# Optimization experiments

Hardware: AMD Instinct MI355X
Metric: run time of the kernel (lower is better)

The kernel has to match this reference:

```python
import jax, jax.numpy as jnp
import numpy as np

WINDOW_SIZES = (4, 16, 64)
MEMORY_DIM = 256


def setup_inputs() -> dict:
    key = jax.random.key(0)
    ks = jax.random.split(key, 9)
    d_model, mem = 256, MEMORY_DIM
    s_in = 1.0 / np.sqrt(d_model)
    s_mem = 1.0 / np.sqrt(mem)
    return {
        "hidden_states": jax.random.normal(ks[0], (2, 4096, d_model), dtype=jnp.float32),
        # weights stored as (in, out) so projection is x @ W + b
        "Wq": jax.random.normal(ks[1], (d_model, mem), dtype=jnp.float32) * s_in,
        "bq": jax.random.normal(ks[2], (mem,), dtype=jnp.float32) * 0.02,
        "Wk": jax.random.normal(ks[3], (d_model, mem), dtype=jnp.float32) * s_in,
        "bk": jax.random.normal(ks[4], (mem,), dtype=jnp.float32) * 0.02,
        "Wv": jax.random.normal(ks[5], (d_model, mem), dtype=jnp.float32) * s_in,
        "bv": jax.random.normal(ks[6], (mem,), dtype=jnp.float32) * 0.02,
        "Wo": jax.random.normal(ks[7], (mem, d_model), dtype=jnp.float32) * s_mem,
        "bo": jax.random.normal(ks[8], (d_model,), dtype=jnp.float32) * 0.02,
    }


def _gather_patches(h, window):
    # h: (B, L, D). Causal window of `window` positions ending at each l,
    # zero-padded on the left (matches F.pad + unfold in the torch module).
    B, L, D = h.shape
    w = min(window, L)
    padded = jnp.pad(h, ((0, 0), (w - 1, 0), (0, 0)))  # (B, L+w-1, D)
    idx = jnp.arange(L)[:, None] + jnp.arange(w)[None, :]  # (L, w)
    return padded[:, idx]  # (B, L, w, D)


def reference(hidden_states, Wq, bq, Wk, bk, Wv, bv, Wo, bo):
    scale = 1.0 / np.sqrt(MEMORY_DIM)
    q = hidden_states @ Wq + bq  # (B, L, M)
    contexts = []
    for window in WINDOW_SIZES:
        patches = _gather_patches(hidden_states, window)  # (B, L, w, D)
        keys = patches @ Wk + bk      # (B, L, w, M)
        values = patches @ Wv + bv    # (B, L, w, M)
        scores = jnp.einsum('bld,blwd->blw', q, keys) * scale
        attn = jax.nn.softmax(scores, axis=-1)
        contexts.append(jnp.einsum('blw,blwd->bld', attn, values))
    merged = contexts[0]
    for c in contexts[1:]:
        merged = merged + c
    merged = merged / len(contexts)
    return hidden_states + merged @ Wo + bo
```

## Files before the change

### kernel.cpp

```cpp
#include <hip/hip_runtime.h>
#include <hip/hip_bf16.h>

#define D 256
#define NROWS 8192
#define LXV 4176
#define VPAD 64
#define KXFB 1064960

#define QBLK 16
#define SSTR 84
#define PSTR 104
#define MSTR 264
#define BSTR 264

typedef unsigned int u32;
typedef unsigned short u16;

typedef short bf16x8 __attribute__((ext_vector_type(8)));
typedef float f32x4 __attribute__((ext_vector_type(4)));

__device__ __forceinline__ u16 f2bf(float f) {
    u32 x = __float_as_uint(f);
    x += 0x7fffu + ((x >> 16) & 1u);
    return (u16)(x >> 16);
}
__device__ __forceinline__ u32 pk2(float a, float b) {
    return (u32)f2bf(a) | ((u32)f2bf(b) << 16);
}

__global__ __launch_bounds__(256) void qkv_mfma(
    const float* __restrict__ H,
    const float* __restrict__ Wq, const float* __restrict__ Wk,
    const float* __restrict__ Wv, const float* __restrict__ Wo,
    const float* __restrict__ bq, const float* __restrict__ bkb,
    const float* __restrict__ bvb,
    u16* __restrict__ Qf, u16* __restrict__ Kxf, u16* __restrict__ Vt,
    u16* __restrict__ WoTf)
{
    __shared__ u16 As[64 * 256];
    __shared__ u16 Bs[64 * BSTR];
    __shared__ u16 Eb[64 * 72];

    const int tid = threadIdx.x;
    const int bx = blockIdx.x;
    const int by = blockIdx.y;
    const int mat = bx >> 2;
    const int n0 = (bx & 3) * 64;
    const int row0 = by * 256;
    const int batch = by >> 4;
    const int lrow0 = row0 & 4095;
    const float* __restrict__ W = (mat == 0) ? Wq : (mat == 1) ? Wk : Wv;
    const float* __restrict__ bias = (mat == 0) ? bq : (mat == 1) ? bkb : bvb;

    const int lane = tid & 63, w = tid >> 6;
    const int l15 = lane & 15, lhi = lane >> 4;
    const int rt2 = (w & 1) * 2, ct2 = (w >> 1) * 2;

    {
        const int kp = tid & 31, ng = tid >> 5;
        u32* bd = (u32*)Bs;
        #pragma unroll
        for (int s = 0; s < 4; ++s) {
            const float* wr = W + (size_t)(s * 64 + 2 * kp) * 256 + n0 + ng * 8;
            float4 a0 = *(const float4*)(wr);
            float4 a1 = *(const float4*)(wr + 4);
            float4 b0 = *(const float4*)(wr + 256);
            float4 b1 = *(const float4*)(wr + 260);
            bd[(ng * 8 + 0) * 132 + s * 32 + kp] = pk2(a0.x, b0.x);
            bd[(ng * 8 + 1) * 132 + s * 32 + kp] = pk2(a0.y, b0.y);
            bd[(ng * 8 + 2) * 132 + s * 32 + kp] = pk2(a0.z, b0.z);
            bd[(ng * 8 + 3) * 132 + s * 32 + kp] = pk2(a0.w, b0.w);
            bd[(ng * 8 + 4) * 132 + s * 32 + kp] = pk2(a1.x, b1.x);
            bd[(ng * 8 + 5) * 132 + s * 32 + kp] = pk2(a1.y, b1.y);
            bd[(ng * 8 + 6) * 132 + s * 32 + kp] = pk2(a1.z, b1.z);
            bd[(ng * 8 + 7) * 132 + s * 32 + kp] = pk2(a1.w, b1.w);
        }
    }
    {
        const int r = tid >> 2, cb = (tid & 3) * 64;
        const float* hp = H + (size_t)(row0 + r) * 256 + cb;
        const int swz = (r & 7) << 3;
        #pragma unroll
        for (int i = 0; i < 16; ++i) {
            float4 h4 = *(const float4*)(hp + i * 4);
            uint2 pv; pv.x = pk2(h4.x, h4.y); pv.y = pk2(h4.z, h4.w);
            *(uint2*)(As + ((r * 256 + cb + i * 4) ^ swz)) = pv;
        }
    }
    __syncthreads();

    for (int t = 0; t < 4; ++t) {
        f32x4 acc[2][2];
        #pragma unroll
        for (int rr = 0; rr < 2; ++rr)
            #pragma unroll
            for (int cc = 0; cc < 2; ++cc)
                acc[rr][cc] = (f32x4){0.f, 0.f, 0.f, 0.f};
        #pragma unroll
        for (int rr = 0; rr < 2; ++rr) {
            const int rowa = (rt2 + rr) * 16 + l15;
            const int swa = (rowa & 7) << 3;
            bf16x8 af[8];
            #pragma unroll
            for (int ks = 0; ks < 8; ++ks)
                af[ks] = *(const bf16x8*)(As + ((rowa * 256 + ks * 32 + lhi * 8) ^ swa));
            #pragma unroll
            for (int ks = 0; ks < 8; ++ks)
                #pragma unroll
                for (int cc = 0; cc < 2; ++cc) {
                    bf16x8 bf = *(const bf16x8*)&Bs[((ct2 + cc) * 16 + l15) * BSTR + ks * 32 + lhi * 8];
                    acc[rr][cc] = __builtin_amdgcn_mfma_f32_16x16x32_bf16(af[ks], bf, acc[rr][cc], 0, 0, 0);
                }
        }
        __syncthreads();

        if (mat == 2) {
            #pragma unroll
            for (int cc = 0; cc < 2; ++cc) {
                const int dl = (ct2 + cc) * 16 + l15;
                const float bi = bvb[n0 + dl];
                #pragma unroll
                for (int rr = 0; rr < 2; ++rr)
                    #pragma unroll
                    for (int reg = 0; reg < 4; ++reg)
                        Eb[dl * 72 + (rt2 + rr) * 16 + lhi * 4 + reg] = f2bf(acc[rr][cc][reg] + bi);
            }
        } else {
            #pragma unroll
            for (int cc = 0; cc < 2; ++cc) {
                const int cl = (ct2 + cc) * 16 + l15;
                const float bi = bias[n0 + cl];
                #pragma unroll
                for (int rr = 0; rr < 2; ++rr)
                    #pragma unroll
                    for (int reg = 0; reg < 4; ++reg)
                        Eb[((rt2 + rr) * 16 + lhi * 4 + reg) * 72 + cl] = f2bf(acc[rr][cc][reg] + bi);
            }
        }
        if (t < 3) {
            const int r = tid >> 2, cb = (tid & 3) * 64;
            const float* hp = H + (size_t)(row0 + (t + 1) * 64 + r) * 256 + cb;
            const int swz = (r & 7) << 3;
            #pragma unroll
            for (int i = 0; i < 16; ++i) {
                float4 h4 = *(const float4*)(hp + i * 4);
                uint2 pv; pv.x = pk2(h4.x, h4.y); pv.y = pk2(h4.z, h4.w);
                *(uint2*)(As + ((r * 256 + cb + i * 4) ^ swz)) = pv;
            }
        }
        __syncthreads();

        if (mat == 2) {
            const int d2 = tid >> 2, q = tid & 3;
            uint4 v0 = *(const uint4*)&Eb[d2 * 72 + q * 16];
            uint4 v1 = *(const uint4*)&Eb[d2 * 72 + q * 16 + 8];
            u16* dst = Vt + ((size_t)batch * 256 + n0 + d2) * LXV + VPAD + lrow0 + t * 64 + q * 16;
            *(uint4*)dst = v0;
            *(uint4*)(dst + 8) = v1;
        } else {
            const int r2 = tid >> 2, c16 = (tid & 3) * 16;
            int rtile, rl;
            u16* base;
            if (mat == 0) {
                const int grow = row0 + t * 64 + r2;
                rtile = grow >> 4; rl = grow & 15;
                base = Qf;
            } else {
                const int prow = VPAD + lrow0 + t * 64 + r2;
                rtile = prow >> 4; rl = prow & 15;
                base = Kxf + (size_t)batch * KXFB;
            }
            #pragma unroll
            for (int h = 0; h < 2; ++h) {
                const int gcol = n0 + c16 + h * 8;
                const int ksq = gcol >> 5;
                const int lhq = (gcol >> 3) & 3;
                uint4 v = *(const uint4*)&Eb[r2 * 72 + c16 + h * 8];
                *(uint4*)&base[((size_t)rtile * 8 + ksq) * 512 + (rl * 4 + lhq) * 8] = v;
            }
        }
    }

    if (bx == 0 && by < 16) {
        float* Tf = (float*)As;
        const int tr = by >> 2, tc = by & 3;
        __syncthreads();
        {
            const int r = tid >> 2, c0 = (tid & 3) * 16;
            const float* src = Wo + (size_t)(tr * 64 + r) * 256 + tc * 64 + c0;
            #pragma unroll
            for (int i = 0; i < 4; ++i) {
                float4 v = *(const float4*)(src + i * 4);
                Tf[r * 68 + c0 + i * 4 + 0] = v.x;
                Tf[r * 68 + c0 + i * 4 + 1] = v.y;
                Tf[r * 68 + c0 + i * 4 + 2] = v.z;
                Tf[r * 68 + c0 + i * 4 + 3] = v.w;
            }
        }
        __syncthreads();
        {
            const int n = tid >> 2, k0 = (tid & 3) * 16;
            const int gcol = tc * 64 + n;
            const int colt = gcol >> 4, cl = gcol & 15;
            const int gk = tr * 64 + k0;
            const int ksw = gk >> 5;
            const int lhw = (gk >> 3) & 3;
            u32 pw[8];
            #pragma unroll
            for (int i = 0; i < 8; ++i)
                pw[i] = pk2(Tf[(k0 + 2 * i) * 68 + n], Tf[(k0 + 2 * i + 1) * 68 + n]);
            u16* base = WoTf + ((size_t)colt * 8 + ksw) * 512 + (cl * 4 + lhw) * 8;
            *(uint4*)base = *(uint4*)&pw[0];
            *(uint4*)(base + 8) = *(uint4*)&pw[4];
        }
    }
    if (bx == 4 && (by & 15) == 0) {
        const int batch2 = by >> 4;
        const int ks = tid >> 5, u = tid & 31;
        const u16 val = f2bf(bkb[ks * 32 + u]);
        u16* base = Kxf + (size_t)batch2 * KXFB;
        #pragma unroll
        for (int pt = 0; pt < 4; ++pt)
            #pragma unroll
            for (int rl = 0; rl < 16; ++rl)
                base[((size_t)pt * 8 + ks) * 512 + rl * 32 + u] = val;
    }
    if (bx == 8 && (by & 15) == 0) {
        const int batch2 = by >> 4;
        const u16 val = f2bf(bvb[tid]);
        const u32 vv = (u32)val | ((u32)val << 16);
        uint4 o; o.x = vv; o.y = vv; o.z = vv; o.w = vv;
        u16* dst = Vt + ((size_t)batch2 * 256 + tid) * LXV;
        #pragma unroll
        for (int j = 0; j < 8; ++j) *(uint4*)(dst + j * 8) = o;
    }
}

__global__ __launch_bounds__(256) void attn_out(
    const u16* __restrict__ Qf, const u16* __restrict__ Kxf,
    const u16* __restrict__ Vt, const u16* __restrict__ WoTf,
    const float* __restrict__ bo, const float* __restrict__ H,
    float* __restrict__ out)
{
    __shared__ float Sb[QBLK * SSTR];
    __shared__ u16 Pb[QBLK * PSTR];
    __shared__ u16 Ml[QBLK * MSTR];

    const int tid = threadIdx.x;
    const int lane = tid & 63, w = tid >> 6;
    const int l15 = lane & 15, lhi = lane >> 4;
    const int r0 = blockIdx.x * QBLK;
    const int batch = r0 >> 12;
    const int lb0 = r0 & 4095;

    const float scale = 0.0625f;
    const int fidx = (l15 * 4 + lhi) * 8;
    const u16* qp = Qf + (size_t)(r0 >> 4) * 4096 + fidx;
    bf16x8 qf[8];
    #pragma unroll
    for (int ks = 0; ks < 8; ++ks) qf[ks] = *(const bf16x8*)(qp + ks * 512);

    const u16* kfb = Kxf + (size_t)batch * KXFB + (size_t)(lb0 >> 4) * 4096 + fidx;
    for (int T = w; T < 5; T += 4) {
        const u16* kp = kfb + (size_t)T * 4096;
        f32x4 acc = (f32x4){0.f, 0.f, 0.f, 0.f};
        #pragma unroll
        for (int ks = 0; ks < 8; ++ks) {
            bf16x8 kf = *(const bf16x8*)(kp + ks * 512);
            acc = __builtin_amdgcn_mfma_f32_16x16x32_bf16(qf[ks], kf, acc, 0, 0, 0);
        }
        #pragma unroll
        for (int reg = 0; reg < 4; ++reg)
            Sb[(lhi * 4 + reg) * SSTR + T * 16 + l15] = acc[reg] * scale;
    }
    __syncthreads();

    {
        const int ri = w * 4 + lhi;
        const int jb = l15;
        float s5[5];
        float m = -1e30f;
        #pragma unroll
        for (int c = 0; c < 5; ++c) {
            const int j = jb + 16 * c;
            const float x = Sb[ri * SSTR + j];
            const bool v = (j >= ri + 1) && (j <= ri + 64);
            s5[c] = v ? x : -1e30f;
            m = fmaxf(m, s5[c]);
        }
        #pragma unroll
        for (int o = 1; o < 16; o <<= 1) m = fmaxf(m, __shfl_xor(m, o));
        float e5[5], z64 = 0.f, z16 = 0.f, z4 = 0.f;
        #pragma unroll
        for (int c = 0; c < 5; ++c) {
            const int j = jb + 16 * c;
            const float e = __expf(s5[c] - m);
            e5[c] = e;
            z64 += e;
            if (j >= ri + 49) z16 += e;
            if (j >= ri + 61) z4 += e;
        }
        #pragma unroll
        for (int o = 1; o < 16; o <<= 1) {
            z64 += __shfl_xor(z64, o);
            z16 += __shfl_xor(z16, o);
            z4  += __shfl_xor(z4, o);
        }
        const float i64 = 1.f / z64, i16 = 1.f / z16, i4 = 1.f / z4;
        #pragma unroll
        for (int c = 0; c < 5; ++c) {
            const int j = jb + 16 * c;
            float wt = e5[c] * (i64 + (j >= ri + 49 ? i16 : 0.f) + (j >= ri + 61 ? i4 : 0.f)) * (1.f / 3.f);
            Pb[ri * PSTR + j] = f2bf(wt);
        }
        Pb[ri * PSTR + 80 + jb] = 0;
    }
    __syncthreads();

    bf16x8 pa[3];
    #pragma unroll
    for (int ks = 0; ks < 3; ++ks)
        pa[ks] = *(const bf16x8*)&Pb[l15 * PSTR + ks * 32 + lhi * 8];
    #pragma unroll
    for (int i = 0; i < 4; ++i) {
        const int dt = w * 4 + i;
        const u16* vrow = Vt + ((size_t)batch * 256 + dt * 16 + l15) * LXV + lb0;
        f32x4 acc = (f32x4){0.f, 0.f, 0.f, 0.f};
        #pragma unroll
        for (int ks = 0; ks < 3; ++ks) {
            bf16x8 vb = *(const bf16x8*)(vrow + ks * 32 + lhi * 8);
            acc = __builtin_amdgcn_mfma_f32_16x16x32_bf16(pa[ks], vb, acc, 0, 0, 0);
        }
        #pragma unroll
        for (int reg = 0; reg < 4; ++reg)
            Ml[(lhi * 4 + reg) * MSTR + dt * 16 + l15] = f2bf(acc[reg]);
    }
    __syncthreads();

    bf16x8 afm[8];
    #pragma unroll
    for (int ks = 0; ks < 8; ++ks)
        afm[ks] = *(const bf16x8*)&Ml[l15 * MSTR + ks * 32 + lhi * 8];

    #pragma unroll
    for (int ct = 0; ct < 4; ++ct) {
        const int colt = w * 4 + ct;
        const u16* wrow = WoTf + (size_t)colt * 4096 + fidx;
        f32x4 oac = (f32x4){0.f, 0.f, 0.f, 0.f};
        #pragma unroll
        for (int ks = 0; ks < 8; ++ks) {
            bf16x8 bf = *(const bf16x8*)(wrow + ks * 512);
            oac = __builtin_amdgcn_mfma_f32_16x16x32_bf16(afm[ks], bf, oac, 0, 0, 0);
        }
        const int col = w * 64 + ct * 16 + l15;
        const float bi = bo[col];
        #pragma unroll
        for (int reg = 0; reg < 4; ++reg) {
            const int r = r0 + lhi * 4 + reg;
            const size_t off = (size_t)r * 256 + col;
            out[off] = H[off] + oac[reg] + bi;
        }
    }
}

extern "C" void kernel_launch(void* const* d_in, const int* in_sizes, int n_in,
                              void* d_out, int out_size, void* d_ws, size_t ws_size,
                              hipStream_t stream) {
    const float* H  = (const float*)d_in[0];
    const float* Wq = (const float*)d_in[1];
    const float* bq = (const float*)d_in[2];
    const float* Wk = (const float*)d_in[3];
    const float* bk = (const float*)d_in[4];
    const float* Wv = (const float*)d_in[5];
    const float* bv = (const float*)d_in[6];
    const float* Wo = (const float*)d_in[7];
    const float* bo = (const float*)d_in[8];
    float* out = (float*)d_out;

    u16* Qf   = (u16*)d_ws;
    u16* Kxf  = Qf + (size_t)NROWS * 256;
    u16* Vt   = Kxf + (size_t)2 * KXFB;
    u16* WoTf = Vt + (size_t)2 * 256 * LXV;

    qkv_mfma<<<dim3(12, 32), 256, 0, stream>>>(H, Wq, Wk, Wv, Wo, bq, bk, bv, Qf, Kxf, Vt, WoTf);
    attn_out<<<512, 256, 0, stream>>>(Qf, Kxf, Vt, WoTf, bo, H, out);
}
```

Baseline: 47.88 us.

## Fold Wo into value projection so attention output skips final GEMM

Precomputes Wvo = Wv·Wo and bvo = bv·Wo in a new small prep kernel. The QKV kernel then projects values directly into output space (U = H·Wvo + bvo), so the attention kernel's P·U result is the output delta. This removes the per-block merged-context staging and the 256x256 output GEMM from the attention kernel. In exchange it adds a serial 4-block prep launch and changes rounding, since the combined weight is rounded to bf16 once.

```diff
diff --git a/kernel.cpp b/kernel.cpp
--- a/kernel.cpp
+++ b/kernel.cpp
@@ -10,7 +10,6 @@
 #define QBLK 16
 #define SSTR 84
 #define PSTR 104
-#define MSTR 264
 #define BSTR 264
 
 typedef unsigned int u32;
@@ -28,14 +27,111 @@
     return (u32)f2bf(a) | ((u32)f2bf(b) << 16);
 }
 
+__global__ __launch_bounds__(256) void wvo_prep(
+    const float* __restrict__ Wv, const float* __restrict__ Wo,
+    const float* __restrict__ bv,
+    float* __restrict__ Wvo, float* __restrict__ bvo)
+{
+    __shared__ u16 As[64 * 256];
+    __shared__ u16 Bs[64 * BSTR];
+    __shared__ float red[256];
+
+    const int tid = threadIdx.x;
+    const int bx = blockIdx.x;
+    const int n0 = bx * 64;
+
+    {
+        const int j = tid & 63, p = tid >> 6;
+        float part = 0.f;
+        for (int m = p * 64; m < p * 64 + 64; ++m)
+            part += bv[m] * Wo[(size_t)m * 256 + n0 + j];
+        red[p * 64 + j] = part;
+    }
+    {
+        const int kp = tid & 31, ng = tid >> 5;
+        u32* bd = (u32*)Bs;
+        #pragma unroll
+        for (int s = 0; s < 4; ++s) {
+            const float* wr = Wo + (size_t)(s * 64 + 2 * kp) * 256 + n0 + ng * 8;
+            float4 a0 = *(const float4*)(wr);
+            float4 a1 = *(const float4*)(wr + 4);
+            float4 b0 = *(const float4*)(wr + 256);
+            float4 b1 = *(const float4*)(wr + 260);
+            bd[(ng * 8 + 0) * 132 + s * 32 + kp] = pk2(a0.x, b0.x);
+            bd[(ng * 8 + 1) * 132 + s * 32 + kp] = pk2(a0.y, b0.y);
+            bd[(ng * 8 + 2) * 132 + s * 32 + kp] = pk2(a0.z, b0.z);
+            bd[(ng * 8 + 3) * 132 + s * 32 + kp] = pk2(a0.w, b0.w);
+            bd[(ng * 8 + 4) * 132 + s * 32 + kp] = pk2(a1.x, b1.x);
+            bd[(ng * 8 + 5) * 132 + s * 32 + kp] = pk2(a1.y, b1.y);
+            bd[(ng * 8 + 6) * 132 + s * 32 + kp] = pk2(a1.z, b1.z);
+            bd[(ng * 8 + 7) * 132 + s * 32 + kp] = pk2(a1.w, b1.w);
+        }
+    }
+    __syncthreads();
+    if (tid < 64)
+        bvo[n0 + tid] = red[tid] + red[64 + tid] + red[128 + tid] + red[192 + tid];
+
+    const int lane = tid & 63, w = tid >> 6;
+    const int l15 = lane & 15, lhi = lane >> 4;
+    const int rt2 = (w & 1) * 2, ct2 = (w >> 1) * 2;
+
+    for (int t = 0; t < 4; ++t) {
+        {
+            const int r = tid >> 2, cb = (tid & 3) * 64;
+            const float* hp = Wv + (size_t)(t * 64 + r) * 256 + cb;
+            const int swz = (r & 7) << 3;
+            #pragma unroll
+            for (int i = 0; i < 16; ++i) {
+                float4 h4 = *(const float4*)(hp + i * 4);
+                uint2 pv; pv.x = pk2(h4.x, h4.y); pv.y = pk2(h4.z, h4.w);
+                *(uint2*)(As + ((r * 256 + cb + i * 4) ^ swz)) = pv;
+            }
+        }
+        __syncthreads();
+
+        f32x4 acc[2][2];
+        #pragma unroll
+        for (int rr = 0; rr < 2; ++rr)
+            #pragma unroll
+            for (int cc = 0; cc < 2; ++cc)
+                acc[rr][cc] = (f32x4){0.f, 0.f, 0.f, 0.f};
+        #pragma unroll
+        for (int rr = 0; rr < 2; ++rr) {
+            const int rowa = (rt2 + rr) * 16 + l15;
+            const int swa = (rowa & 7) << 3;
+            bf16x8 af[8];
+            #pragma unroll
+            for (int ks = 0; ks < 8; ++ks)
+                af[ks] = *(const bf16x8*)(As + ((rowa * 256 + ks * 32 + lhi * 8) ^ swa));
+            #pragma unroll
+            for (int ks = 0; ks < 8; ++ks)
+                #pragma unroll
+                for (int cc = 0; cc < 2; ++cc) {
+                    bf16x8 bf = *(const bf16x8*)&Bs[((ct2 + cc) * 16 + l15) * BSTR + ks * 32 + lhi * 8];
+                    acc[rr][cc] = __builtin_amdgcn_mfma_f32_16x16x32_bf16(af[ks], bf, acc[rr][cc], 0, 0, 0);
+                }
+        }
+        #pragma unroll
+        for (int rr = 0; rr < 2; ++rr)
+            #pragma unroll
+            for (int cc = 0; cc < 2; ++cc)
+                #pragma unroll
+                for (int reg = 0; reg < 4; ++reg) {
+                    const int row = t * 64 + (rt2 + rr) * 16 + lhi * 4 + reg;
+                    const int col = n0 + (ct2 + cc) * 16 + l15;
+                    Wvo[(size_t)row * 256 + col] = acc[rr][cc][reg];
+                }
+        __syncthreads();
+    }
+}
+
 __global__ __launch_bounds__(256) void qkv_mfma(
     const float* __restrict__ H,
     const float* __restrict__ Wq, const float* __restrict__ Wk,
-    const float* __restrict__ Wv, const float* __restrict__ Wo,
+    const float* __restrict__ Wvo,
     const float* __restrict__ bq, const float* __restrict__ bkb,
-    const float* __restrict__ bvb,
-    u16* __restrict__ Qf, u16* __restrict__ Kxf, u16* __restrict__ Vt,
-    u16* __restrict__ WoTf)
+    const float* __restrict__ bvo,
+    u16* __restrict__ Qf, u16* __restrict__ Kxf, u16* __restrict__ Ut)
 {
     __shared__ u16 As[64 * 256];
     __shared__ u16 Bs[64 * BSTR];
@@ -49,8 +145,8 @@
     const int row0 = by * 256;
     const int batch = by >> 4;
     const int lrow0 = row0 & 4095;
-    const float* __restrict__ W = (mat == 0) ? Wq : (mat == 1) ? Wk : Wv;
-    const float* __restrict__ bias = (mat == 0) ? bq : (mat == 1) ? bkb : bvb;
+    const float* __restrict__ W = (mat == 0) ? Wq : (mat == 1) ? Wk : Wvo;
+    const float* __restrict__ bias = (mat == 0) ? bq : (mat == 1) ? bkb : bvo;
 
     const int lane = tid & 63, w = tid >> 6;
     const int l15 = lane & 15, lhi = lane >> 4;
@@ -118,7 +214,7 @@
             #pragma unroll
             for (int cc = 0; cc < 2; ++cc) {
                 const int dl = (ct2 + cc) * 16 + l15;
-                const float bi = bvb[n0 + dl];
+                const float bi = bias[n0 + dl];
                 #pragma unroll
                 for (int rr = 0; rr < 2; ++rr)
                     #pragma unroll
@@ -154,7 +250,7 @@
             const int d2 = tid >> 2, q = tid & 3;
             uint4 v0 = *(const uint4*)&Eb[d2 * 72 + q * 16];
             uint4 v1 = *(const uint4*)&Eb[d2 * 72 + q * 16 + 8];
-            u16* dst = Vt + ((size_t)batch * 256 + n0 + d2) * LXV + VPAD + lrow0 + t * 64 + q * 16;
+            u16* dst = Ut + ((size_t)batch * 256 + n0 + d2) * LXV + VPAD + lrow0 + t * 64 + q * 16;
             *(uint4*)dst = v0;
             *(uint4*)(dst + 8) = v1;
         } else {
@@ -181,39 +277,6 @@
         }
     }
 
-    if (bx == 0 && by < 16) {
-        float* Tf = (float*)As;
-        const int tr = by >> 2, tc = by & 3;
-        __syncthreads();
-        {
-            const int r = tid >> 2, c0 = (tid & 3) * 16;
-            const float* src = Wo + (size_t)(tr * 64 + r) * 256 + tc * 64 + c0;
-            #pragma unroll
-            for (int i = 0; i < 4; ++i) {
-                float4 v = *(const float4*)(src + i * 4);
-                Tf[r * 68 + c0 + i * 4 + 0] = v.x;
-                Tf[r * 68 + c0 + i * 4 + 1] = v.y;
-                Tf[r * 68 + c0 + i * 4 + 2] = v.z;
-                Tf[r * 68 + c0 + i * 4 + 3] = v.w;
-            }
-        }
-        __syncthreads();
-        {
-            const int n = tid >> 2, k0 = (tid & 3) * 16;
-            const int gcol = tc * 64 + n;
-            const int colt = gcol >> 4, cl = gcol & 15;
-            const int gk = tr * 64 + k0;
-            const int ksw = gk >> 5;
-            const int lhw = (gk >> 3) & 3;
-            u32 pw[8];
-            #pragma unroll
-            for (int i = 0; i < 8; ++i)
-                pw[i] = pk2(Tf[(k0 + 2 * i) * 68 + n], Tf[(k0 + 2 * i + 1) * 68 + n]);
-            u16* base = WoTf + ((size_t)colt * 8 + ksw) * 512 + (cl * 4 + lhw) * 8;
-            *(uint4*)base = *(uint4*)&pw[0];
-            *(uint4*)(base + 8) = *(uint4*)&pw[4];
-        }
-    }
     if (bx == 4 && (by & 15) == 0) {
         const int batch2 = by >> 4;
         const int ks = tid >> 5, u = tid & 31;
@@ -227,10 +290,10 @@
     }
     if (bx == 8 && (by & 15) == 0) {
         const int batch2 = by >> 4;
-        const u16 val = f2bf(bvb[tid]);
+        const u16 val = f2bf(bvo[tid]);
         const u32 vv = (u32)val | ((u32)val << 16);
         uint4 o; o.x = vv; o.y = vv; o.z = vv; o.w = vv;
-        u16* dst = Vt + ((size_t)batch2 * 256 + tid) * LXV;
+        u16* dst = Ut + ((size_t)batch2 * 256 + tid) * LXV;
         #pragma unroll
         for (int j = 0; j < 8; ++j) *(uint4*)(dst + j * 8) = o;
     }
@@ -238,13 +301,11 @@
 
 __global__ __launch_bounds__(256) void attn_out(
     const u16* __restrict__ Qf, const u16* __restrict__ Kxf,
-    const u16* __restrict__ Vt, const u16* __restrict__ WoTf,
-    const float* __restrict__ bo, const float* __restrict__ H,
-    float* __restrict__ out)
+    const u16* __restrict__ Ut, const float* __restrict__ bo,
+    const float* __restrict__ H, float* __restrict__ out)
 {
     __shared__ float Sb[QBLK * SSTR];
     __shared__ u16 Pb[QBLK * PSTR];
-    __shared__ u16 Ml[QBLK * MSTR];
 
     const int tid = threadIdx.x;
     const int lane = tid & 63, w = tid >> 6;
@@ -324,41 +385,20 @@
     #pragma unroll
     for (int i = 0; i < 4; ++i) {
         const int dt = w * 4 + i;
-        const u16* vrow = Vt + ((size_t)batch * 256 + dt * 16 + l15) * LXV + lb0;
+        const u16* urow = Ut + ((size_t)batch * 256 + dt * 16 + l15) * LXV + lb0;
         f32x4 acc = (f32x4){0.f, 0.f, 0.f, 0.f};
         #pragma unroll
         for (int ks = 0; ks < 3; ++ks) {
-            bf16x8 vb = *(const bf16x8*)(vrow + ks * 32 + lhi * 8);
-            acc = __builtin_amdgcn_mfma_f32_16x16x32_bf16(pa[ks], vb, acc, 0, 0, 0);
-        }
-        #pragma unroll
-        for (int reg = 0; reg < 4; ++reg)
-            Ml[(lhi * 4 + reg) * MSTR + dt * 16 + l15] = f2bf(acc[reg]);
-    }
-    __syncthreads();
-
-    bf16x8 afm[8];
-    #pragma unroll
-    for (int ks = 0; ks < 8; ++ks)
-        afm[ks] = *(const bf16x8*)&Ml[l15 * MSTR + ks * 32 + lhi * 8];
-
-    #pragma unroll
-    for (int ct = 0; ct < 4; ++ct) {
-        const int colt = w * 4 + ct;
-        const u16* wrow = WoTf + (size_t)colt * 4096 + fidx;
-        f32x4 oac = (f32x4){0.f, 0.f, 0.f, 0.f};
-        #pragma unroll
-        for (int ks = 0; ks < 8; ++ks) {
-            bf16x8 bf = *(const bf16x8*)(wrow + ks * 512);
-            oac = __builtin_amdgcn_mfma_f32_16x16x32_bf16(afm[ks], bf, oac, 0, 0, 0);
-        }
-        const int col = w * 64 + ct * 16 + l15;
+            bf16x8 ub = *(const bf16x8*)(urow + ks * 32 + lhi * 8);
+            acc = __builtin_amdgcn_mfma_f32_16x16x32_bf16(pa[ks], ub, acc, 0, 0, 0);
+        }
+        const int col = dt * 16 + l15;
         const float bi = bo[col];
         #pragma unroll
         for (int reg = 0; reg < 4; ++reg) {
             const int r = r0 + lhi * 4 + reg;
             const size_t off = (size_t)r * 256 + col;
-            out[off] = H[off] + oac[reg] + bi;
+            out[off] = H[off] + acc[reg] + bi;
         }
     }
 }
@@ -379,9 +419,11 @@
 
     u16* Qf   = (u16*)d_ws;
     u16* Kxf  = Qf + (size_t)NROWS * 256;
-    u16* Vt   = Kxf + (size_t)2 * KXFB;
-    u16* WoTf = Vt + (size_t)2 * 256 * LXV;
-
-    qkv_mfma<<<dim3(12, 32), 256, 0, stream>>>(H, Wq, Wk, Wv, Wo, bq, bk, bv, Qf, Kxf, Vt, WoTf);
-    attn_out<<<512, 256, 0, stream>>>(Qf, Kxf, Vt, WoTf, bo, H, out);
-}
+    u16* Ut   = Kxf + (size_t)2 * KXFB;
+    float* Wvo = (float*)(Ut + (size_t)2 * 256 * LXV);
+    float* bvo = Wvo + 256 * 256;
+
+    wvo_prep<<<4, 256, 0, stream>>>(Wv, Wo, bv, Wvo, bvo);
+    qkv_mfma<<<dim3(12, 32), 256, 0, stream>>>(H, Wq, Wk, Wvo, bq, bk, bvo, Qf, Kxf, Ut);
+    attn_out<<<512, 256, 0, stream>>>(Qf, Kxf, Ut, bo, H, out);
+}
```

New measurement: 77.34 us. 1.62x slower.
